# Kernel optimization log

Measured on AMD Instinct MI355X. Metric: run time of the kernel, lower is better.

Reference implementation:

```python
import jax, jax.numpy as jnp
import numpy as np

N_NODES = 100000
N_EDGES = 1600000
C_IN, C_HID, C_OUT = 64, 64, 32


def _gcn_conv(x, src, dst, ew, W, b, n_nodes):
    """PyG GCNConv: add self-loops (weight 1), symmetric normalization,
    out[dst] += norm * (x @ W)[src], plus bias. Dropout omitted (eval mode)."""
    h = x @ W  # [N, C_out_layer]
    loop = jnp.arange(n_nodes, dtype=src.dtype)
    src_a = jnp.concatenate([src, loop])
    dst_a = jnp.concatenate([dst, loop])
    ew_a = jnp.concatenate([ew, jnp.ones((n_nodes,), dtype=ew.dtype)])
    # degree over incoming (dst) side, weighted
    deg = jax.ops.segment_sum(ew_a, dst_a, num_segments=n_nodes)
    dinv = jnp.where(deg > 0, jax.lax.rsqrt(deg), 0.0)
    norm = dinv[src_a] * ew_a * dinv[dst_a]  # [E+N]
    msg = h[src_a] * norm[:, None]           # gather + scale: [E+N, C]
    out = jax.ops.segment_sum(msg, dst_a, num_segments=n_nodes)  # scatter-add
    return out + b


def setup_inputs() -> dict:
    key = jax.random.key(0)
    k1, k2, k3, k4, k5, k6, k7 = jax.random.split(key, 7)
    x = jax.random.normal(k1, (N_NODES, C_IN), dtype=jnp.float32)
    edge_index = jax.random.randint(k2, (2, N_EDGES), 0, N_NODES, dtype=jnp.int64)
    edge_attr = jax.random.uniform(k3, (N_EDGES,), dtype=jnp.float32)
    s1 = 1.0 / np.sqrt(C_IN)
    s2 = 1.0 / np.sqrt(C_HID)
    W1 = jax.random.uniform(k4, (C_IN, C_HID), jnp.float32, -s1, s1)
    b1 = jnp.zeros((C_HID,), dtype=jnp.float32)
    W2 = jax.random.uniform(k5, (C_HID, C_OUT), jnp.float32, -s2, s2)
    b2 = jnp.zeros((C_OUT,), dtype=jnp.float32)
    return {"x": x, "edge_index": edge_index, "edge_attr": edge_attr,
            "W1": W1, "b1": b1, "W2": W2, "b2": b2}


def reference(x, edge_index, edge_attr, W1, b1, W2, b2):
    n = x.shape[0]
    src, dst = edge_index[0], edge_index[1]
    h = _gcn_conv(x, src, dst, edge_attr, W1, b1, n)
    h = jax.nn.relu(h)  # dropout is identity in eval mode
    out = _gcn_conv(h, src, dst, edge_attr, W2, b2, n)
    return out
```

## Files before the change

kernel.cpp:

```cpp
#include <hip/hip_runtime.h>
#include <hip/hip_fp16.h>


#define TPB 256
#define TPB_P 512
#define TPB_S 1024
#define BSH2 8
#define BN2 256
#define NBC 512
#define PCHUNK 4096
#define CAP2 5632
#define XSTR 68

typedef union { uint2 u; __half2 h[2]; } hpack;
typedef union { uint4 u; __half2 h[4]; } hpack8;

__device__ __forceinline__ int enc_w(float w) {
  unsigned b = __float_as_uint(w);
  return (int)(((b + 0x7FFFu + ((b >> 16) & 1u)) >> 16) & 0x7FFFu);
}
__device__ __forceinline__ float dec_w(int e) {
  return __uint_as_float(((unsigned)e >> 17) << 16);
}

__global__ __launch_bounds__(TPB_P) void k_part(const int* __restrict__ si,
                                                const int* __restrict__ di,
                                                const float* __restrict__ ew,
                                                int* __restrict__ bpos,
                                                int2* __restrict__ tin, int e) {
  __shared__ int hcnt[NBC];
  __shared__ int lst0[NBC];
  __shared__ int lcur[NBC];
  __shared__ int hbase[NBC];
  __shared__ int2 se[PCHUNK];
  __shared__ unsigned short sbk[PCHUNK];
  int t = threadIdx.x;
  int lo = blockIdx.x * PCHUNK;
  int hi = lo + PCHUNK; if (hi > e) hi = e;
  int cn = hi - lo;
  hcnt[t] = 0;
  __syncthreads();
  for (int i = lo + t; i < hi; i += TPB_P) atomicAdd(&hcnt[di[i] >> BSH2], 1);
  __syncthreads();
  int c = hcnt[t];
  for (int off = 1; off < NBC; off <<= 1) {
    int u = (t >= off) ? hcnt[t - off] : 0;
    __syncthreads();
    hcnt[t] += u;
    __syncthreads();
  }
  {
    int ex = hcnt[t] - c;
    lst0[t] = ex;
    lcur[t] = 0;
    hbase[t] = c ? (t * CAP2 + atomicAdd(&bpos[t], c)) : 0;
  }
  __syncthreads();
  for (int i = lo + t; i < hi; i += TPB_P) {
    int d = di[i];
    int bk = d >> BSH2;
    int loc = atomicAdd(&lcur[bk], 1);
    int p = lst0[bk] + loc;
    se[p] = make_int2(si[i] | ((d & (BN2 - 1)) << 17), __float_as_int(ew[i]));
    sbk[p] = (unsigned short)bk;
  }
  __syncthreads();
  for (int p = t; p < cn; p += TPB_P) {
    int bk = sbk[p];
    tin[hbase[bk] + (p - lst0[bk])] = se[p];
  }
}

__global__ __launch_bounds__(TPB_S) void k_sortb(const int2* __restrict__ tin,
                                                 const int* __restrict__ bpos,
                                                 int* __restrict__ colpk,
                                                 int2* __restrict__ rowseg,
                                                 float* __restrict__ dinv, int n) {
  __shared__ int cnt[BN2];
  __shared__ float degw[BN2];
  __shared__ int cur[BN2];
  __shared__ int ls[BN2];
  __shared__ int2 se[PCHUNK];
  int b = blockIdx.x, t = threadIdx.x;
  if (t < BN2) { cnt[t] = 0; degw[t] = 1.0f; }
  __syncthreads();
  int jb = b * CAP2, je = jb + bpos[b];
  for (int j = jb + t; j < je; j += TPB_S) {
    int2 p = tin[j];
    int o = j - jb;
    if (o < PCHUNK) se[o] = p;
    int dl = p.x >> 17;
    atomicAdd(&cnt[dl], 1);
    atomicAdd(&degw[dl], __int_as_float(p.y));
  }
  __syncthreads();
  int c = (t < BN2) ? cnt[t] : 0;
  int c4 = (c + 3) & ~3;
  if (t < BN2) ls[t] = c4;
  __syncthreads();
  for (int off = 1; off < BN2; off <<= 1) {
    int u = (t >= off && t < BN2) ? ls[t - off] : 0;
    __syncthreads();
    if (t < BN2) ls[t] += u;
    __syncthreads();
  }
  int base = b << BSH2;
  if (t < BN2) {
    int start = jb + ls[t] - c4;
    cur[t] = start;
    int node = base + t;
    if (node < n) {
      rowseg[node] = make_int2(start, start + c4);
      dinv[node] = rsqrtf(degw[t]);
    }
    for (int i = c; i < c4; ++i) colpk[start + i] = 0;
  }
  __syncthreads();
  for (int j = jb + t; j < je; j += TPB_S) {
    int o = j - jb;
    int2 p = (o < PCHUNK) ? se[o] : tin[j];
    int dl = p.x >> 17;
    int pos = atomicAdd(&cur[dl], 1);
    colpk[pos] = (p.x & 0x1FFFF) | (enc_w(__int_as_float(p.y)) << 17);
  }
}

__global__ __launch_bounds__(TPB) void k_gemm1(const float* __restrict__ x,
                                               const float* __restrict__ W1,
                                               const float* __restrict__ dinv,
                                               __half* __restrict__ g1h, int n) {
  __shared__ float Wl[64 * 64];
  int t = threadIdx.x;
  {
    const float4* W4 = (const float4*)W1;
    float4* Wl4 = (float4*)Wl;
#pragma unroll
    for (int i = 0; i < 4; ++i) Wl4[t + TPB * i] = W4[t + TPB * i];
  }
  __syncthreads();
  int r = blockIdx.x * 16 + (t >> 4);
  if (r >= n) return;
  int c0 = (t & 15) << 2;
  const float4* xr = (const float4*)(x + (size_t)r * 64);
  float ax = 0.f, ay = 0.f, az = 0.f, aw = 0.f;
#pragma unroll
  for (int kk = 0; kk < 16; ++kk) {
    float4 xv = xr[kk];
    const float* w = &Wl[(kk * 4) * 64 + c0];
    float4 w0 = *(const float4*)(w);
    float4 w1 = *(const float4*)(w + 64);
    float4 w2 = *(const float4*)(w + 128);
    float4 w3 = *(const float4*)(w + 192);
    ax += xv.x * w0.x + xv.y * w1.x + xv.z * w2.x + xv.w * w3.x;
    ay += xv.x * w0.y + xv.y * w1.y + xv.z * w2.y + xv.w * w3.y;
    az += xv.x * w0.z + xv.y * w1.z + xv.z * w2.z + xv.w * w3.z;
    aw += xv.x * w0.w + xv.y * w1.w + xv.z * w2.w + xv.w * w3.w;
  }
  float dv = dinv[r];
  hpack pk;
  pk.h[0] = __floats2half2_rn(dv * ax, dv * ay);
  pk.h[1] = __floats2half2_rn(dv * az, dv * aw);
  *(uint2*)(g1h + (size_t)r * 64 + c0) = pk.u;
}

__global__ __launch_bounds__(TPB) void k_gfuse(const __half* __restrict__ g1h,
                                               const int* __restrict__ colpk,
                                               const int2* __restrict__ rowseg,
                                               const float* __restrict__ dinv,
                                               const float* __restrict__ W2,
                                               const float* __restrict__ b1,
                                               __half* __restrict__ g2h, int n) {
  __shared__ float W2l[64 * 32];
  __shared__ float b1l[64];
  __shared__ float x2l[32 * XSTR];
  int t = threadIdx.x;
  {
    const float4* W4 = (const float4*)W2;
    float4* Wl4 = (float4*)W2l;
#pragma unroll
    for (int i = 0; i < 2; ++i) Wl4[t + TPB * i] = W4[t + TPB * i];
    if (t < 64) b1l[t] = b1[t];
  }
  __syncthreads();
  int node = t >> 3;
  int r = blockIdx.x * 32 + node;
  int c0 = (t & 7) << 3;
  bool valid = (r < n);
  float a[8];
  float dv = 0.f;
  if (valid) {
    dv = dinv[r];
    hpack8 s; s.u = *(const uint4*)(g1h + (size_t)r * 64 + c0);
#pragma unroll
    for (int k = 0; k < 4; ++k) {
      float2 f = __half22float2(s.h[k]);
      a[2 * k] = f.x; a[2 * k + 1] = f.y;
    }
    int2 seg = rowseg[r];
    int j = seg.x;
    for (; j + 7 < seg.y; j += 8) {
      int4 qa = *(const int4*)(colpk + j);
      int4 qb = *(const int4*)(colpk + j + 4);
      hpack8 u0; u0.u = *(const uint4*)(g1h + (size_t)(qa.x & 0x1FFFF) * 64 + c0);
      hpack8 u1; u1.u = *(const uint4*)(g1h + (size_t)(qa.y & 0x1FFFF) * 64 + c0);
      hpack8 u2; u2.u = *(const uint4*)(g1h + (size_t)(qa.z & 0x1FFFF) * 64 + c0);
      hpack8 u3; u3.u = *(const uint4*)(g1h + (size_t)(qa.w & 0x1FFFF) * 64 + c0);
      hpack8 u4; u4.u = *(const uint4*)(g1h + (size_t)(qb.x & 0x1FFFF) * 64 + c0);
      hpack8 u5; u5.u = *(const uint4*)(g1h + (size_t)(qb.y & 0x1FFFF) * 64 + c0);
      hpack8 u6; u6.u = *(const uint4*)(g1h + (size_t)(qb.z & 0x1FFFF) * 64 + c0);
      hpack8 u7; u7.u = *(const uint4*)(g1h + (size_t)(qb.w & 0x1FFFF) * 64 + c0);
      float w0 = dec_w(qa.x), w1 = dec_w(qa.y), w2 = dec_w(qa.z), w3 = dec_w(qa.w);
      float w4 = dec_w(qb.x), w5 = dec_w(qb.y), w6 = dec_w(qb.z), w7 = dec_w(qb.w);
#pragma unroll
      for (int k = 0; k < 4; ++k) {
        float2 f;
        f = __half22float2(u0.h[k]); a[2*k] += w0 * f.x; a[2*k+1] += w0 * f.y;
        f = __half22float2(u1.h[k]); a[2*k] += w1 * f.x; a[2*k+1] += w1 * f.y;
        f = __half22float2(u2.h[k]); a[2*k] += w2 * f.x; a[2*k+1] += w2 * f.y;
        f = __half22float2(u3.h[k]); a[2*k] += w3 * f.x; a[2*k+1] += w3 * f.y;
        f = __half22float2(u4.h[k]); a[2*k] += w4 * f.x; a[2*k+1] += w4 * f.y;
        f = __half22float2(u5.h[k]); a[2*k] += w5 * f.x; a[2*k+1] += w5 * f.y;
        f = __half22float2(u6.h[k]); a[2*k] += w6 * f.x; a[2*k+1] += w6 * f.y;
        f = __half22float2(u7.h[k]); a[2*k] += w7 * f.x; a[2*k+1] += w7 * f.y;
      }
    }
    if (j < seg.y) {
      int4 qa = *(const int4*)(colpk + j);
      hpack8 u0; u0.u = *(const uint4*)(g1h + (size_t)(qa.x & 0x1FFFF) * 64 + c0);
      hpack8 u1; u1.u = *(const uint4*)(g1h + (size_t)(qa.y & 0x1FFFF) * 64 + c0);
      hpack8 u2; u2.u = *(const uint4*)(g1h + (size_t)(qa.z & 0x1FFFF) * 64 + c0);
      hpack8 u3; u3.u = *(const uint4*)(g1h + (size_t)(qa.w & 0x1FFFF) * 64 + c0);
      float w0 = dec_w(qa.x), w1 = dec_w(qa.y), w2 = dec_w(qa.z), w3 = dec_w(qa.w);
#pragma unroll
      for (int k = 0; k < 4; ++k) {
        float2 f;
        f = __half22float2(u0.h[k]); a[2*k] += w0 * f.x; a[2*k+1] += w0 * f.y;
        f = __half22float2(u1.h[k]); a[2*k] += w1 * f.x; a[2*k+1] += w1 * f.y;
        f = __half22float2(u2.h[k]); a[2*k] += w2 * f.x; a[2*k+1] += w2 * f.y;
        f = __half22float2(u3.h[k]); a[2*k] += w3 * f.x; a[2*k+1] += w3 * f.y;
      }
    }
    float* xp = x2l + node * XSTR + c0;
#pragma unroll
    for (int k = 0; k < 8; k += 4) {
      float4 v = {fmaxf(dv * a[k + 0] + b1l[c0 + k + 0], 0.f),
                  fmaxf(dv * a[k + 1] + b1l[c0 + k + 1], 0.f),
                  fmaxf(dv * a[k + 2] + b1l[c0 + k + 2], 0.f),
                  fmaxf(dv * a[k + 3] + b1l[c0 + k + 3], 0.f)};
      *(float4*)(xp + k) = v;
    }
  }
  __syncthreads();
  if (!valid) return;
  int oc = (t & 7) << 2;
  const float* xr = x2l + node * XSTR;
  float ax = 0.f, ay = 0.f, az = 0.f, aw = 0.f;
#pragma unroll
  for (int kk = 0; kk < 16; ++kk) {
    float4 xv = *(const float4*)(xr + 4 * kk);
    const float* w = &W2l[(kk * 4) * 32 + oc];
    float4 w0 = *(const float4*)(w);
    float4 w1 = *(const float4*)(w + 32);
    float4 w2 = *(const float4*)(w + 64);
    float4 w3 = *(const float4*)(w + 96);
    ax += xv.x * w0.x + xv.y * w1.x + xv.z * w2.x + xv.w * w3.x;
    ay += xv.x * w0.y + xv.y * w1.y + xv.z * w2.y + xv.w * w3.y;
    az += xv.x * w0.z + xv.y * w1.z + xv.z * w2.z + xv.w * w3.z;
    aw += xv.x * w0.w + xv.y * w1.w + xv.z * w2.w + xv.w * w3.w;
  }
  hpack pk;
  pk.h[0] = __floats2half2_rn(dv * ax, dv * ay);
  pk.h[1] = __floats2half2_rn(dv * az, dv * aw);
  *(uint2*)(g2h + (size_t)r * 32 + oc) = pk.u;
}

__global__ __launch_bounds__(TPB) void k_gather32(const __half* __restrict__ g2h,
                                                  const int* __restrict__ colpk,
                                                  const int2* __restrict__ rowseg,
                                                  const float* __restrict__ dinv,
                                                  const float* __restrict__ b2,
                                                  float* __restrict__ out, int n) {
  int t = threadIdx.x;
  int r = blockIdx.x * 64 + (t >> 2);
  if (r >= n) return;
  int c0 = (t & 3) << 3;
  float a[8];
  {
    hpack8 s; s.u = *(const uint4*)(g2h + (size_t)r * 32 + c0);
#pragma unroll
    for (int k = 0; k < 4; ++k) {
      float2 f = __half22float2(s.h[k]);
      a[2 * k] = f.x; a[2 * k + 1] = f.y;
    }
  }
  int2 seg = rowseg[r];
  int j = seg.x;
  for (; j + 7 < seg.y; j += 8) {
    int4 qa = *(const int4*)(colpk + j);
    int4 qb = *(const int4*)(colpk + j + 4);
    hpack8 u0; u0.u = *(const uint4*)(g2h + (size_t)(qa.x & 0x1FFFF) * 32 + c0);
    hpack8 u1; u1.u = *(const uint4*)(g2h + (size_t)(qa.y & 0x1FFFF) * 32 + c0);
    hpack8 u2; u2.u = *(const uint4*)(g2h + (size_t)(qa.z & 0x1FFFF) * 32 + c0);
    hpack8 u3; u3.u = *(const uint4*)(g2h + (size_t)(qa.w & 0x1FFFF) * 32 + c0);
    hpack8 u4; u4.u = *(const uint4*)(g2h + (size_t)(qb.x & 0x1FFFF) * 32 + c0);
    hpack8 u5; u5.u = *(const uint4*)(g2h + (size_t)(qb.y & 0x1FFFF) * 32 + c0);
    hpack8 u6; u6.u = *(const uint4*)(g2h + (size_t)(qb.z & 0x1FFFF) * 32 + c0);
    hpack8 u7; u7.u = *(const uint4*)(g2h + (size_t)(qb.w & 0x1FFFF) * 32 + c0);
    float w0 = dec_w(qa.x), w1 = dec_w(qa.y), w2 = dec_w(qa.z), w3 = dec_w(qa.w);
    float w4 = dec_w(qb.x), w5 = dec_w(qb.y), w6 = dec_w(qb.z), w7 = dec_w(qb.w);
#pragma unroll
    for (int k = 0; k < 4; ++k) {
      float2 f;
      f = __half22float2(u0.h[k]); a[2*k] += w0 * f.x; a[2*k+1] += w0 * f.y;
      f = __half22float2(u1.h[k]); a[2*k] += w1 * f.x; a[2*k+1] += w1 * f.y;
      f = __half22float2(u2.h[k]); a[2*k] += w2 * f.x; a[2*k+1] += w2 * f.y;
      f = __half22float2(u3.h[k]); a[2*k] += w3 * f.x; a[2*k+1] += w3 * f.y;
      f = __half22float2(u4.h[k]); a[2*k] += w4 * f.x; a[2*k+1] += w4 * f.y;
      f = __half22float2(u5.h[k]); a[2*k] += w5 * f.x; a[2*k+1] += w5 * f.y;
      f = __half22float2(u6.h[k]); a[2*k] += w6 * f.x; a[2*k+1] += w6 * f.y;
      f = __half22float2(u7.h[k]); a[2*k] += w7 * f.x; a[2*k+1] += w7 * f.y;
    }
  }
  if (j < seg.y) {
    int4 qa = *(const int4*)(colpk + j);
    hpack8 u0; u0.u = *(const uint4*)(g2h + (size_t)(qa.x & 0x1FFFF) * 32 + c0);
    hpack8 u1; u1.u = *(const uint4*)(g2h + (size_t)(qa.y & 0x1FFFF) * 32 + c0);
    hpack8 u2; u2.u = *(const uint4*)(g2h + (size_t)(qa.z & 0x1FFFF) * 32 + c0);
    hpack8 u3; u3.u = *(const uint4*)(g2h + (size_t)(qa.w & 0x1FFFF) * 32 + c0);
    float w0 = dec_w(qa.x), w1 = dec_w(qa.y), w2 = dec_w(qa.z), w3 = dec_w(qa.w);
#pragma unroll
    for (int k = 0; k < 4; ++k) {
      float2 f;
      f = __half22float2(u0.h[k]); a[2*k] += w0 * f.x; a[2*k+1] += w0 * f.y;
      f = __half22float2(u1.h[k]); a[2*k] += w1 * f.x; a[2*k+1] += w1 * f.y;
      f = __half22float2(u2.h[k]); a[2*k] += w2 * f.x; a[2*k+1] += w2 * f.y;
      f = __half22float2(u3.h[k]); a[2*k] += w3 * f.x; a[2*k+1] += w3 * f.y;
    }
  }
  float dv = dinv[r];
  const float4* b24 = (const float4*)(b2 + c0);
  float4 bb0 = b24[0], bb1 = b24[1];
  float* op = out + (size_t)r * 32 + c0;
  *(float4*)(op)     = make_float4(dv * a[0] + bb0.x, dv * a[1] + bb0.y,
                                   dv * a[2] + bb0.z, dv * a[3] + bb0.w);
  *(float4*)(op + 4) = make_float4(dv * a[4] + bb1.x, dv * a[5] + bb1.y,
                                   dv * a[6] + bb1.z, dv * a[7] + bb1.w);
}

extern "C" void kernel_launch(void* const* d_in, const int* in_sizes, int n_in,
                              void* d_out, int out_size, void* d_ws, size_t ws_size,
                              hipStream_t stream) {
  const float* x  = (const float*)d_in[0];
  const int* ei   = (const int*)d_in[1];
  const float* ew = (const float*)d_in[2];
  const float* W1 = (const float*)d_in[3];
  const float* b1 = (const float*)d_in[4];
  const float* W2 = (const float*)d_in[5];
  const float* b2 = (const float*)d_in[6];
  float* out = (float*)d_out;

  const int n = in_sizes[0] / 64;
  const int e = in_sizes[1] / 2;
  const int* si = ei;
  const int* di = ei + e;
  const int NBc = (n + BN2 - 1) >> BSH2;

  float* ws = (float*)d_ws;
  const size_t NP = 100352;
  const size_t SLOTS = (size_t)NBc * CAP2;
  float*  dinv   = ws;
  __half* g1h    = (__half*)(ws + NP);
  int2*   rowseg = (int2*)(ws + NP + (size_t)n * 32);
  int*    bpos   = (int*)(rowseg + NP);
  int*    colpk  = bpos + 1024;
  int2*   tin    = (int2*)(colpk + SLOTS);
  __half* g2h    = (__half*)(tin + SLOTS);

  int gb_part = (e + PCHUNK - 1) / PCHUNK;
  int gb_g1 = (n + 15) / 16;
  int gb_gf = (n + 31) / 32;
  int gb_g32 = (n + 63) / 64;

  hipMemsetAsync(bpos, 0, NBC * sizeof(int), stream);
  k_part<<<gb_part, TPB_P, 0, stream>>>(si, di, ew, bpos, tin, e);
  k_sortb<<<NBc, TPB_S, 0, stream>>>(tin, bpos, colpk, rowseg, dinv, n);
  k_gemm1<<<gb_g1, TPB, 0, stream>>>(x, W1, dinv, g1h, n);
  k_gfuse<<<gb_gf, TPB, 0, stream>>>(g1h, colpk, rowseg, dinv, W2, b1, g2h, n);
  k_gather32<<<gb_g32, TPB, 0, stream>>>(g2h, colpk, rowseg, dinv, b2, out, n);
}
```

Measured before the change: 205.7 us.

## Merge layer-1 GEMM into edge partition kernel and apply source dinv per edge

Measured after the change: 203.3 us, median of 2. Within noise of the previous version (-1.2%).

```diff
diff --git a/kernel.cpp b/kernel.cpp
--- a/kernel.cpp
+++ b/kernel.cpp
@@ -23,51 +23,88 @@
   return __uint_as_float(((unsigned)e >> 17) << 16);
 }
 
-__global__ __launch_bounds__(TPB_P) void k_part(const int* __restrict__ si,
-                                                const int* __restrict__ di,
-                                                const float* __restrict__ ew,
-                                                int* __restrict__ bpos,
-                                                int2* __restrict__ tin, int e) {
-  __shared__ int hcnt[NBC];
-  __shared__ int lst0[NBC];
-  __shared__ int lcur[NBC];
-  __shared__ int hbase[NBC];
-  __shared__ int2 se[PCHUNK];
-  __shared__ unsigned short sbk[PCHUNK];
+__global__ __launch_bounds__(TPB_P) void k_fat(const int* __restrict__ si,
+                                               const int* __restrict__ di,
+                                               const float* __restrict__ ew,
+                                               int* __restrict__ bpos,
+                                               int2* __restrict__ tin,
+                                               const float* __restrict__ x,
+                                               const float* __restrict__ W1,
+                                               __half* __restrict__ h1h,
+                                               int e, int n, int gbp) {
+  __shared__ union SM {
+    struct {
+      int hcnt[NBC]; int lst0[NBC]; int lcur[NBC]; int hbase[NBC];
+      int2 se[PCHUNK]; unsigned short sbk[PCHUNK];
+    } p;
+    float Wl[64 * 64];
+  } sm;
   int t = threadIdx.x;
-  int lo = blockIdx.x * PCHUNK;
-  int hi = lo + PCHUNK; if (hi > e) hi = e;
-  int cn = hi - lo;
-  hcnt[t] = 0;
-  __syncthreads();
-  for (int i = lo + t; i < hi; i += TPB_P) atomicAdd(&hcnt[di[i] >> BSH2], 1);
-  __syncthreads();
-  int c = hcnt[t];
-  for (int off = 1; off < NBC; off <<= 1) {
-    int u = (t >= off) ? hcnt[t - off] : 0;
-    __syncthreads();
-    hcnt[t] += u;
-    __syncthreads();
-  }
-  {
-    int ex = hcnt[t] - c;
-    lst0[t] = ex;
-    lcur[t] = 0;
-    hbase[t] = c ? (t * CAP2 + atomicAdd(&bpos[t], c)) : 0;
-  }
-  __syncthreads();
-  for (int i = lo + t; i < hi; i += TPB_P) {
-    int d = di[i];
-    int bk = d >> BSH2;
-    int loc = atomicAdd(&lcur[bk], 1);
-    int p = lst0[bk] + loc;
-    se[p] = make_int2(si[i] | ((d & (BN2 - 1)) << 17), __float_as_int(ew[i]));
-    sbk[p] = (unsigned short)bk;
-  }
-  __syncthreads();
-  for (int p = t; p < cn; p += TPB_P) {
-    int bk = sbk[p];
-    tin[hbase[bk] + (p - lst0[bk])] = se[p];
+  if (blockIdx.x < (unsigned)gbp) {
+    int lo = blockIdx.x * PCHUNK;
+    int hi = lo + PCHUNK; if (hi > e) hi = e;
+    int cn = hi - lo;
+    sm.p.hcnt[t] = 0;
+    __syncthreads();
+    for (int i = lo + t; i < hi; i += TPB_P) atomicAdd(&sm.p.hcnt[di[i] >> BSH2], 1);
+    __syncthreads();
+    int c = sm.p.hcnt[t];
+    for (int off = 1; off < NBC; off <<= 1) {
+      int u = (t >= off) ? sm.p.hcnt[t - off] : 0;
+      __syncthreads();
+      sm.p.hcnt[t] += u;
+      __syncthreads();
+    }
+    {
+      int ex = sm.p.hcnt[t] - c;
+      sm.p.lst0[t] = ex;
+      sm.p.lcur[t] = 0;
+      sm.p.hbase[t] = c ? (t * CAP2 + atomicAdd(&bpos[t], c)) : 0;
+    }
+    __syncthreads();
+    for (int i = lo + t; i < hi; i += TPB_P) {
+      int d = di[i];
+      int bk = d >> BSH2;
+      int loc = atomicAdd(&sm.p.lcur[bk], 1);
+      int p = sm.p.lst0[bk] + loc;
+      sm.p.se[p] = make_int2(si[i] | ((d & (BN2 - 1)) << 17), __float_as_int(ew[i]));
+      sm.p.sbk[p] = (unsigned short)bk;
+    }
+    __syncthreads();
+    for (int p = t; p < cn; p += TPB_P) {
+      int bk = sm.p.sbk[p];
+      tin[sm.p.hbase[bk] + (p - sm.p.lst0[bk])] = sm.p.se[p];
+    }
+  } else {
+    {
+      const float4* W4 = (const float4*)W1;
+      float4* Wl4 = (float4*)sm.Wl;
+#pragma unroll
+      for (int i = 0; i < 2; ++i) Wl4[t + TPB_P * i] = W4[t + TPB_P * i];
+    }
+    __syncthreads();
+    int r = (blockIdx.x - gbp) * 32 + (t >> 4);
+    if (r >= n) return;
+    int c0 = (t & 15) << 2;
+    const float4* xr = (const float4*)(x + (size_t)r * 64);
+    float ax = 0.f, ay = 0.f, az = 0.f, aw = 0.f;
+#pragma unroll
+    for (int kk = 0; kk < 16; ++kk) {
+      float4 xv = xr[kk];
+      const float* w = &sm.Wl[(kk * 4) * 64 + c0];
+      float4 w0 = *(const float4*)(w);
+      float4 w1 = *(const float4*)(w + 64);
+      float4 w2 = *(const float4*)(w + 128);
+      float4 w3 = *(const float4*)(w + 192);
+      ax += xv.x * w0.x + xv.y * w1.x + xv.z * w2.x + xv.w * w3.x;
+      ay += xv.x * w0.y + xv.y * w1.y + xv.z * w2.y + xv.w * w3.y;
+      az += xv.x * w0.z + xv.y * w1.z + xv.z * w2.z + xv.w * w3.z;
+      aw += xv.x * w0.w + xv.y * w1.w + xv.z * w2.w + xv.w * w3.w;
+    }
+    hpack pk;
+    pk.h[0] = __floats2half2_rn(ax, ay);
+    pk.h[1] = __floats2half2_rn(az, aw);
+    *(uint2*)(h1h + (size_t)r * 64 + c0) = pk.u;
   }
 }
 
@@ -123,44 +160,6 @@
     int pos = atomicAdd(&cur[dl], 1);
     colpk[pos] = (p.x & 0x1FFFF) | (enc_w(__int_as_float(p.y)) << 17);
   }
-}
-
-__global__ __launch_bounds__(TPB) void k_gemm1(const float* __restrict__ x,
-                                               const float* __restrict__ W1,
-                                               const float* __restrict__ dinv,
-                                               __half* __restrict__ g1h, int n) {
-  __shared__ float Wl[64 * 64];
-  int t = threadIdx.x;
-  {
-    const float4* W4 = (const float4*)W1;
-    float4* Wl4 = (float4*)Wl;
-#pragma unroll
-    for (int i = 0; i < 4; ++i) Wl4[t + TPB * i] = W4[t + TPB * i];
-  }
-  __syncthreads();
-  int r = blockIdx.x * 16 + (t >> 4);
-  if (r >= n) return;
-  int c0 = (t & 15) << 2;
-  const float4* xr = (const float4*)(x + (size_t)r * 64);
-  float ax = 0.f, ay = 0.f, az = 0.f, aw = 0.f;
-#pragma unroll
-  for (int kk = 0; kk < 16; ++kk) {
-    float4 xv = xr[kk];
-    const float* w = &Wl[(kk * 4) * 64 + c0];
-    float4 w0 = *(const float4*)(w);
-    float4 w1 = *(const float4*)(w + 64);
-    float4 w2 = *(const float4*)(w + 128);
-    float4 w3 = *(const float4*)(w + 192);
-    ax += xv.x * w0.x + xv.y * w1.x + xv.z * w2.x + xv.w * w3.x;
-    ay += xv.x * w0.y + xv.y * w1.y + xv.z * w2.y + xv.w * w3.y;
-    az += xv.x * w0.z + xv.y * w1.z + xv.z * w2.z + xv.w * w3.z;
-    aw += xv.x * w0.w + xv.y * w1.w + xv.z * w2.w + xv.w * w3.w;
-  }
-  float dv = dinv[r];
-  hpack pk;
-  pk.h[0] = __floats2half2_rn(dv * ax, dv * ay);
-  pk.h[1] = __floats2half2_rn(dv * az, dv * aw);
-  *(uint2*)(g1h + (size_t)r * 64 + c0) = pk.u;
 }
 
 __global__ __launch_bounds__(TPB) void k_gfuse(const __half* __restrict__ g1h,
@@ -194,23 +193,27 @@
 #pragma unroll
     for (int k = 0; k < 4; ++k) {
       float2 f = __half22float2(s.h[k]);
-      a[2 * k] = f.x; a[2 * k + 1] = f.y;
+      a[2 * k] = dv * f.x; a[2 * k + 1] = dv * f.y;
     }
     int2 seg = rowseg[r];
     int j = seg.x;
     for (; j + 7 < seg.y; j += 8) {
       int4 qa = *(const int4*)(colpk + j);
       int4 qb = *(const int4*)(colpk + j + 4);
-      hpack8 u0; u0.u = *(const uint4*)(g1h + (size_t)(qa.x & 0x1FFFF) * 64 + c0);
-      hpack8 u1; u1.u = *(const uint4*)(g1h + (size_t)(qa.y & 0x1FFFF) * 64 + c0);
-      hpack8 u2; u2.u = *(const uint4*)(g1h + (size_t)(qa.z & 0x1FFFF) * 64 + c0);
-      hpack8 u3; u3.u = *(const uint4*)(g1h + (size_t)(qa.w & 0x1FFFF) * 64 + c0);
-      hpack8 u4; u4.u = *(const uint4*)(g1h + (size_t)(qb.x & 0x1FFFF) * 64 + c0);
-      hpack8 u5; u5.u = *(const uint4*)(g1h + (size_t)(qb.y & 0x1FFFF) * 64 + c0);
-      hpack8 u6; u6.u = *(const uint4*)(g1h + (size_t)(qb.z & 0x1FFFF) * 64 + c0);
-      hpack8 u7; u7.u = *(const uint4*)(g1h + (size_t)(qb.w & 0x1FFFF) * 64 + c0);
-      float w0 = dec_w(qa.x), w1 = dec_w(qa.y), w2 = dec_w(qa.z), w3 = dec_w(qa.w);
-      float w4 = dec_w(qb.x), w5 = dec_w(qb.y), w6 = dec_w(qb.z), w7 = dec_w(qb.w);
+      int s0 = qa.x & 0x1FFFF, s1 = qa.y & 0x1FFFF, s2 = qa.z & 0x1FFFF, s3 = qa.w & 0x1FFFF;
+      int s4 = qb.x & 0x1FFFF, s5 = qb.y & 0x1FFFF, s6 = qb.z & 0x1FFFF, s7 = qb.w & 0x1FFFF;
+      hpack8 u0; u0.u = *(const uint4*)(g1h + (size_t)s0 * 64 + c0);
+      hpack8 u1; u1.u = *(const uint4*)(g1h + (size_t)s1 * 64 + c0);
+      hpack8 u2; u2.u = *(const uint4*)(g1h + (size_t)s2 * 64 + c0);
+      hpack8 u3; u3.u = *(const uint4*)(g1h + (size_t)s3 * 64 + c0);
+      hpack8 u4; u4.u = *(const uint4*)(g1h + (size_t)s4 * 64 + c0);
+      hpack8 u5; u5.u = *(const uint4*)(g1h + (size_t)s5 * 64 + c0);
+      hpack8 u6; u6.u = *(const uint4*)(g1h + (size_t)s6 * 64 + c0);
+      hpack8 u7; u7.u = *(const uint4*)(g1h + (size_t)s7 * 64 + c0);
+      float w0 = dec_w(qa.x) * dinv[s0], w1 = dec_w(qa.y) * dinv[s1];
+      float w2 = dec_w(qa.z) * dinv[s2], w3 = dec_w(qa.w) * dinv[s3];
+      float w4 = dec_w(qb.x) * dinv[s4], w5 = dec_w(qb.y) * dinv[s5];
+      float w6 = dec_w(qb.z) * dinv[s6], w7 = dec_w(qb.w) * dinv[s7];
 #pragma unroll
       for (int k = 0; k < 4; ++k) {
         float2 f;
@@ -226,11 +229,13 @@
     }
     if (j < seg.y) {
       int4 qa = *(const int4*)(colpk + j);
-      hpack8 u0; u0.u = *(const uint4*)(g1h + (size_t)(qa.x & 0x1FFFF) * 64 + c0);
-      hpack8 u1; u1.u = *(const uint4*)(g1h + (size_t)(qa.y & 0x1FFFF) * 64 + c0);
-      hpack8 u2; u2.u = *(const uint4*)(g1h + (size_t)(qa.z & 0x1FFFF) * 64 + c0);
-      hpack8 u3; u3.u = *(const uint4*)(g1h + (size_t)(qa.w & 0x1FFFF) * 64 + c0);
-      float w0 = dec_w(qa.x), w1 = dec_w(qa.y), w2 = dec_w(qa.z), w3 = dec_w(qa.w);
+      int s0 = qa.x & 0x1FFFF, s1 = qa.y & 0x1FFFF, s2 = qa.z & 0x1FFFF, s3 = qa.w & 0x1FFFF;
+      hpack8 u0; u0.u = *(const uint4*)(g1h + (size_t)s0 * 64 + c0);
+      hpack8 u1; u1.u = *(const uint4*)(g1h + (size_t)s1 * 64 + c0);
+      hpack8 u2; u2.u = *(const uint4*)(g1h + (size_t)s2 * 64 + c0);
+      hpack8 u3; u3.u = *(const uint4*)(g1h + (size_t)s3 * 64 + c0);
+      float w0 = dec_w(qa.x) * dinv[s0], w1 = dec_w(qa.y) * dinv[s1];
+      float w2 = dec_w(qa.z) * dinv[s2], w3 = dec_w(qa.w) * dinv[s3];
 #pragma unroll
       for (int k = 0; k < 4; ++k) {
         float2 f;
@@ -269,8 +274,8 @@
     aw += xv.x * w0.w + xv.y * w1.w + xv.z * w2.w + xv.w * w3.w;
   }
   hpack pk;
-  pk.h[0] = __floats2half2_rn(dv * ax, dv * ay);
-  pk.h[1] = __floats2half2_rn(dv * az, dv * aw);
+  pk.h[0] = __floats2half2_rn(ax, ay);
+  pk.h[1] = __floats2half2_rn(az, aw);
   *(uint2*)(g2h + (size_t)r * 32 + oc) = pk.u;
 }
 
@@ -284,13 +289,14 @@
   int r = blockIdx.x * 64 + (t >> 2);
   if (r >= n) return;
   int c0 = (t & 3) << 3;
+  float dv = dinv[r];
   float a[8];
   {
     hpack8 s; s.u = *(const uint4*)(g2h + (size_t)r * 32 + c0);
 #pragma unroll
     for (int k = 0; k < 4; ++k) {
       float2 f = __half22float2(s.h[k]);
-      a[2 * k] = f.x; a[2 * k + 1] = f.y;
+      a[2 * k] = dv * f.x; a[2 * k + 1] = dv * f.y;
     }
   }
   int2 seg = rowseg[r];
@@ -298,16 +304,20 @@
   for (; j + 7 < seg.y; j += 8) {
     int4 qa = *(const int4*)(colpk + j);
     int4 qb = *(const int4*)(colpk + j + 4);
-    hpack8 u0; u0.u = *(const uint4*)(g2h + (size_t)(qa.x & 0x1FFFF) * 32 + c0);
-    hpack8 u1; u1.u = *(const uint4*)(g2h + (size_t)(qa.y & 0x1FFFF) * 32 + c0);
-    hpack8 u2; u2.u = *(const uint4*)(g2h + (size_t)(qa.z & 0x1FFFF) * 32 + c0);
-    hpack8 u3; u3.u = *(const uint4*)(g2h + (size_t)(qa.w & 0x1FFFF) * 32 + c0);
-    hpack8 u4; u4.u = *(const uint4*)(g2h + (size_t)(qb.x & 0x1FFFF) * 32 + c0);
-    hpack8 u5; u5.u = *(const uint4*)(g2h + (size_t)(qb.y & 0x1FFFF) * 32 + c0);
-    hpack8 u6; u6.u = *(const uint4*)(g2h + (size_t)(qb.z & 0x1FFFF) * 32 + c0);
-    hpack8 u7; u7.u = *(const uint4*)(g2h + (size_t)(qb.w & 0x1FFFF) * 32 + c0);
-    float w0 = dec_w(qa.x), w1 = dec_w(qa.y), w2 = dec_w(qa.z), w3 = dec_w(qa.w);
-    float w4 = dec_w(qb.x), w5 = dec_w(qb.y), w6 = dec_w(qb.z), w7 = dec_w(qb.w);
+    int s0 = qa.x & 0x1FFFF, s1 = qa.y & 0x1FFFF, s2 = qa.z & 0x1FFFF, s3 = qa.w & 0x1FFFF;
+    int s4 = qb.x & 0x1FFFF, s5 = qb.y & 0x1FFFF, s6 = qb.z & 0x1FFFF, s7 = qb.w & 0x1FFFF;
+    hpack8 u0; u0.u = *(const uint4*)(g2h + (size_t)s0 * 32 + c0);
+    hpack8 u1; u1.u = *(const uint4*)(g2h + (size_t)s1 * 32 + c0);
+    hpack8 u2; u2.u = *(const uint4*)(g2h + (size_t)s2 * 32 + c0);
+    hpack8 u3; u3.u = *(const uint4*)(g2h + (size_t)s3 * 32 + c0);
+    hpack8 u4; u4.u = *(const uint4*)(g2h + (size_t)s4 * 32 + c0);
+    hpack8 u5; u5.u = *(const uint4*)(g2h + (size_t)s5 * 32 + c0);
+    hpack8 u6; u6.u = *(const uint4*)(g2h + (size_t)s6 * 32 + c0);
+    hpack8 u7; u7.u = *(const uint4*)(g2h + (size_t)s7 * 32 + c0);
+    float w0 = dec_w(qa.x) * dinv[s0], w1 = dec_w(qa.y) * dinv[s1];
+    float w2 = dec_w(qa.z) * dinv[s2], w3 = dec_w(qa.w) * dinv[s3];
+    float w4 = dec_w(qb.x) * dinv[s4], w5 = dec_w(qb.y) * dinv[s5];
+    float w6 = dec_w(qb.z) * dinv[s6], w7 = dec_w(qb.w) * dinv[s7];
 #pragma unroll
     for (int k = 0; k < 4; ++k) {
       float2 f;
@@ -323,11 +333,13 @@
   }
   if (j < seg.y) {
     int4 qa = *(const int4*)(colpk + j);
-    hpack8 u0; u0.u = *(const uint4*)(g2h + (size_t)(qa.x & 0x1FFFF) * 32 + c0);
-    hpack8 u1; u1.u = *(const uint4*)(g2h + (size_t)(qa.y & 0x1FFFF) * 32 + c0);
-    hpack8 u2; u2.u = *(const uint4*)(g2h + (size_t)(qa.z & 0x1FFFF) * 32 + c0);
-    hpack8 u3; u3.u = *(const uint4*)(g2h + (size_t)(qa.w & 0x1FFFF) * 32 + c0);
-    float w0 = dec_w(qa.x), w1 = dec_w(qa.y), w2 = dec_w(qa.z), w3 = dec_w(qa.w);
+    int s0 = qa.x & 0x1FFFF, s1 = qa.y & 0x1FFFF, s2 = qa.z & 0x1FFFF, s3 = qa.w & 0x1FFFF;
+    hpack8 u0; u0.u = *(const uint4*)(g2h + (size_t)s0 * 32 + c0);
+    hpack8 u1; u1.u = *(const uint4*)(g2h + (size_t)s1 * 32 + c0);
+    hpack8 u2; u2.u = *(const uint4*)(g2h + (size_t)s2 * 32 + c0);
+    hpack8 u3; u3.u = *(const uint4*)(g2h + (size_t)s3 * 32 + c0);
+    float w0 = dec_w(qa.x) * dinv[s0], w1 = dec_w(qa.y) * dinv[s1];
+    float w2 = dec_w(qa.z) * dinv[s2], w3 = dec_w(qa.w) * dinv[s3];
 #pragma unroll
     for (int k = 0; k < 4; ++k) {
       float2 f;
@@ -337,7 +349,6 @@
       f = __half22float2(u3.h[k]); a[2*k] += w3 * f.x; a[2*k+1] += w3 * f.y;
     }
   }
-  float dv = dinv[r];
   const float4* b24 = (const float4*)(b2 + c0);
   float4 bb0 = b24[0], bb1 = b24[1];
   float* op = out + (size_t)r * 32 + c0;
@@ -377,14 +388,14 @@
   __half* g2h    = (__half*)(tin + SLOTS);
 
   int gb_part = (e + PCHUNK - 1) / PCHUNK;
-  int gb_g1 = (n + 15) / 16;
+  int gb_g1 = (n + 31) / 32;
   int gb_gf = (n + 31) / 32;
   int gb_g32 = (n + 63) / 64;
 
   hipMemsetAsync(bpos, 0, NBC * sizeof(int), stream);
-  k_part<<<gb_part, TPB_P, 0, stream>>>(si, di, ew, bpos, tin, e);
+  k_fat<<<gb_part + gb_g1, TPB_P, 0, stream>>>(si, di, ew, bpos, tin,
+                                               x, W1, g1h, e, n, gb_part);
   k_sortb<<<NBc, TPB_S, 0, stream>>>(tin, bpos, colpk, rowseg, dinv, n);
-  k_gemm1<<<gb_g1, TPB, 0, stream>>>(x, W1, dinv, g1h, n);
   k_gfuse<<<gb_gf, TPB, 0, stream>>>(g1h, colpk, rowseg, dinv, W2, b1, g2h, n);
   k_gather32<<<gb_g32, TPB, 0, stream>>>(g2h, colpk, rowseg, dinv, b2, out, n);
 }
```
